# Kernel tuning notes

Measured on AMD Instinct MI355X. Metric: run time of the kernel, lower is better.

The kernel has to match this reference:

```python
import jax, jax.numpy as jnp
import numpy as np

B, S, D, H, F = 2, 2048, 768, 12, 3072
HD = D // H


def setup_inputs() -> dict:
    key = jax.random.key(0)
    ks = jax.random.split(key, 6)
    g = lambda k, sh, sc: jax.random.normal(k, sh, jnp.float32) * sc
    return {
        "x": g(ks[0], (B, S, D), 1.0),
        "mask": jnp.tril(jnp.ones((1, 1, S, S), dtype=jnp.bool_)),  # causal
        "qkv_w": g(ks[1], (3 * D, D), 0.02),
        "qkv_b": jnp.zeros((3 * D,), jnp.float32),
        "out_w": g(ks[2], (D, D), 0.02),
        "out_b": jnp.zeros((D,), jnp.float32),
        "fc1_w": g(ks[3], (F, D), 0.02),
        "fc1_b": jnp.zeros((F,), jnp.float32),
        "fc2_w": g(ks[4], (D, F), 0.02),
        "fc2_b": jnp.zeros((D,), jnp.float32),
        "ln1_w": jnp.ones((D,), jnp.float32),
        "ln1_b": jnp.zeros((D,), jnp.float32),
        "ln2_w": jnp.ones((D,), jnp.float32),
        "ln2_b": jnp.zeros((D,), jnp.float32),
    }


def _layernorm(x, w, b, eps=1e-5):
    m = x.mean(-1, keepdims=True)
    v = ((x - m) ** 2).mean(-1, keepdims=True)
    return (x - m) * jax.lax.rsqrt(v + eps) * w + b


def reference(x, mask, qkv_w, qkv_b, out_w, out_b, fc1_w, fc1_b, fc2_w, fc2_b,
              ln1_w, ln1_b, ln2_w, ln2_b):
    b, s, d = x.shape
    h = d // HD  # num_heads
    # --- pre-norm multi-head self-attention (dropout = eval/identity) ---
    hx = _layernorm(x, ln1_w, ln1_b)
    qkv = hx @ qkv_w.T + qkv_b                      # [b,s,3d]
    qkv = qkv.reshape(b, s, 3, h, HD).transpose(2, 0, 3, 1, 4)  # [3,b,h,s,hd]
    q, k, v = qkv[0], qkv[1], qkv[2]
    scale = jnp.sqrt(jnp.float32(HD))
    scores = jnp.einsum("bhqd,bhkd->bhqk", q, k) / scale  # [b,h,s,s]
    scores = jnp.where(mask, scores, -jnp.inf)
    attn = jax.nn.softmax(scores, axis=-1)
    o = jnp.einsum("bhqk,bhkd->bhqd", attn, v)      # [b,h,s,hd]
    o = o.transpose(0, 2, 1, 3).reshape(b, s, d)
    x = x + (o @ out_w.T + out_b)
    # --- pre-norm GELU feed-forward ---
    h2 = _layernorm(x, ln2_w, ln2_b)
    ff = jax.nn.gelu(h2 @ fc1_w.T + fc1_b, approximate=False) @ fc2_w.T + fc2_b
    return x + ff
```

## Files before the change

kernel.cpp:

```cpp
#include <hip/hip_runtime.h>
#include <hip/hip_bf16.h>
#include <cstdint>
#include <cstddef>

typedef __bf16 bf16;
typedef unsigned short ushort_t;
typedef __attribute__((ext_vector_type(8))) __bf16 bf16x8;
typedef __attribute__((ext_vector_type(4))) __bf16 bf16x4;
typedef __attribute__((ext_vector_type(4))) float f32x4;

#define NB 2
#define NS 2048
#define ND 768
#define NH 12
#define NF 3072
#define NT (NB * NS)

__device__ __forceinline__ f32x4 mfma16(bf16x8 a, bf16x8 b, f32x4 c) {
  return __builtin_amdgcn_mfma_f32_16x16x32_bf16(a, b, c, 0, 0, 0);
}

__device__ __forceinline__ void gl_lds16(const bf16* g, bf16* l) {
  __builtin_amdgcn_global_load_lds(
      (__attribute__((address_space(1))) void*)(uintptr_t)g,
      (__attribute__((address_space(3))) void*)l,
      16, 0, 0);
}

__device__ __forceinline__ int xcd_swz(int lin, int nwg) {
  const int q = nwg >> 3, r = nwg & 7;
  const int x = lin & 7, i = lin >> 3;
  return (x < r ? x * (q + 1) : r * (q + 1) + (x - r) * q) + i;
}

__device__ __forceinline__ float gelu_fast(float v) {
  const float u = v * (0.7978845608028654f + 0.03567740814f * v * v);
  const float e = exp2f(u * 2.885390081777927f);
  return v - v / (1.f + e);
}

__global__ __launch_bounds__(256) void sniff_kernel(
    const ushort_t* __restrict__ x, int* __restrict__ flag) {
  __shared__ int s[4];
  int bad = 0;
  for (int i = threadIdx.x; i < 4096; i += 256) {
    const int e = (x[i] >> 7) & 0xFF;
    bad |= (e >= 0xC0);
  }
  bad = __any(bad) ? 1 : 0;
  if ((threadIdx.x & 63) == 0) s[threadIdx.x >> 6] = bad;
  __syncthreads();
  if (threadIdx.x == 0) *flag = s[0] | s[1] | s[2] | s[3];
}

struct CvtArgs {
  const void* s[8];
  bf16* d[8];
  int n8[8];
  int total8;
};

__global__ __launch_bounds__(256) void cvt_all(CvtArgs a,
                                               const int* __restrict__ flag) {
  const int isf = *flag;
  const int stride = gridDim.x * 256;
  for (int i = blockIdx.x * 256 + threadIdx.x; i < a.total8; i += stride) {
    int seg = 0, off = i;
    while (off >= a.n8[seg]) { off -= a.n8[seg]; ++seg; }
    bf16x8 o;
    if (isf) {
      const float* s = (const float*)a.s[seg] + (size_t)off * 8;
      const f32x4 f0 = *(const f32x4*)s;
      const f32x4 f1 = *(const f32x4*)(s + 4);
#pragma unroll
      for (int j = 0; j < 4; ++j) {
        o[j] = (bf16)f0[j];
        o[4 + j] = (bf16)f1[j];
      }
    } else {
      o = *((const bf16x8*)a.s[seg] + off);
    }
    *((bf16x8*)a.d[seg] + off) = o;
  }
}

__global__ __launch_bounds__(256) void ln_kernel(
    const void* __restrict__ xv, const void* __restrict__ wv,
    const void* __restrict__ bv, bf16* __restrict__ y,
    const int* __restrict__ flag) {
  const int isf = *flag;
  const int row = blockIdx.x * 4 + (threadIdx.x >> 6);
  const int L = threadIdx.x & 63;
  const float* xf = (const float*)xv;
  const bf16* xh = (const bf16*)xv;
  const float* wf = (const float*)wv;
  const bf16* wh = (const bf16*)wv;
  const float* bf_ = (const float*)bv;
  const bf16* bh = (const bf16*)bv;
  const size_t base = (size_t)row * ND;
  float v[12];
  float s = 0.f, s2 = 0.f;
#pragma unroll
  for (int i = 0; i < 12; ++i) {
    const int c = L + i * 64;
    v[i] = isf ? xf[base + c] : (float)xh[base + c];
    s += v[i];
    s2 += v[i] * v[i];
  }
#pragma unroll
  for (int off = 1; off < 64; off <<= 1) {
    s += __shfl_xor(s, off);
    s2 += __shfl_xor(s2, off);
  }
  const float mean = s * (1.f / 768.f);
  const float var = s2 * (1.f / 768.f) - mean * mean;
  const float rstd = rsqrtf(var + 1e-5f);
  bf16* yr = y + base;
#pragma unroll
  for (int i = 0; i < 12; ++i) {
    const int c = L + i * 64;
    const float ww = isf ? wf[c] : (float)wh[c];
    const float bb = isf ? bf_[c] : (float)bh[c];
    yr[c] = (bf16)((v[i] - mean) * rstd * ww + bb);
  }
}

__global__ __launch_bounds__(256) void vt_kernel(
    const bf16* __restrict__ qkv, bf16* __restrict__ vT) {
  const int bh = blockIdx.y;
  const int b = bh / NH, h = bh % NH;
  const int st = blockIdx.x;
  __shared__ bf16 Vs[64 * 72];
  const int tid = threadIdx.x;
  {
    const int r = tid >> 2, c = (tid & 3) * 16;
    const bf16* src =
        qkv + (size_t)(b * NS + st * 64 + r) * (3 * ND) + 2 * ND + h * 64 + c;
    *(bf16x8*)&Vs[r * 72 + c] = *(const bf16x8*)src;
    *(bf16x8*)&Vs[r * 72 + c + 8] = *(const bf16x8*)(src + 8);
  }
  __syncthreads();
  {
    const int hd = tid >> 2, t0 = (tid & 3) * 16;
    bf16x8 o0, o1;
#pragma unroll
    for (int j = 0; j < 8; ++j) {
      o0[j] = Vs[(t0 + j) * 72 + hd];
      o1[j] = Vs[(t0 + 8 + j) * 72 + hd];
    }
    bf16* dst = vT + ((size_t)bh * 64 + hd) * NS + st * 64 + t0;
    *(bf16x8*)dst = o0;
    *(bf16x8*)(dst + 8) = o1;
  }
}

template <int EPI, int TM>
__global__ __launch_bounds__(256) void gemm_fast(
    const bf16* __restrict__ A, const bf16* __restrict__ Bt,
    const bf16* __restrict__ bias, const void* resid, void* C,
    int N, int K, int row0, const int* __restrict__ flag) {
  constexpr int NBUF = (TM == 64) ? 5 : 3;
  constexpr int LOOK = NBUF - 2;
  constexpr int MT = TM / 32;
  __shared__ bf16 As[NBUF][TM * 32];
  __shared__ bf16 Bs[NBUF][128 * 32];
  int isf = 0;
  if (EPI == 2) {
    isf = *flag;
    asm volatile("" ::"s"(isf));
  }
  const int tid = threadIdx.x;
  const int w = tid >> 6, L = tid & 63;
  const int lg = L >> 4, lc = L & 15;
  const int lgx = (lg ^ ((lc >> 1) & 3)) * 8;
  const int wm = (w >> 1) * (TM / 2), wn = (w & 1) * 64;
  const int nwg = gridDim.x * gridDim.y;
  const int lin = xcd_swz(blockIdx.y * gridDim.x + blockIdx.x, nwg);
  const int bm = lin / gridDim.x, bn = lin % gridDim.x;

  const bf16* Ab = A + (size_t)bm * TM * K;
  const bf16* Bb = Bt + (size_t)bn * 128 * K;

  const int sr = tid >> 2;
  const int sc = ((tid & 3) ^ ((tid >> 3) & 3)) * 8;

  f32x4 acc[MT][4];
#pragma unroll
  for (int i = 0; i < MT; ++i)
#pragma unroll
    for (int j = 0; j < 4; ++j) acc[i][j] = (f32x4){0.f, 0.f, 0.f, 0.f};

#define GF_STAGE(buf, kk)                                                   \
  do {                                                                      \
    gl_lds16(Ab + (size_t)sr * K + (kk) + sc, As[buf] + tid * 8);           \
    if (TM == 128)                                                          \
      gl_lds16(Ab + (size_t)(sr + 64) * K + (kk) + sc,                      \
               As[buf] + 2048 + tid * 8);                                   \
    gl_lds16(Bb + (size_t)sr * K + (kk) + sc, Bs[buf] + tid * 8);           \
    gl_lds16(Bb + (size_t)(sr + 64) * K + (kk) + sc,                        \
             Bs[buf] + 2048 + tid * 8);                                     \
  } while (0)

#define GF_COMP(cb)                                                         \
  do {                                                                      \
    bf16x8 af[MT], bfr[4];                                                  \
    _Pragma("unroll") for (int mt = 0; mt < MT; ++mt) af[mt] =              \
        *(const bf16x8*)&As[cb][(wm + mt * 16 + lc) * 32 + lgx];            \
    _Pragma("unroll") for (int nt = 0; nt < 4; ++nt) bfr[nt] =              \
        *(const bf16x8*)&Bs[cb][(wn + nt * 16 + lc) * 32 + lgx];            \
    _Pragma("unroll") for (int mt = 0; mt < MT; ++mt)                       \
        _Pragma("unroll") for (int nt = 0; nt < 4; ++nt) acc[mt][nt] =      \
            mfma16(af[mt], bfr[nt], acc[mt][nt]);                           \
  } while (0)

  const int nk = K >> 5;
#pragma unroll
  for (int s = 0; s < LOOK; ++s)
    if (s < nk) GF_STAGE(s, s * 32);
  int cur = 0, stg = LOOK;
  int k = 0;
  const int kmain = (nk > LOOK) ? nk - LOOK : 0;
  for (; k < kmain; ++k) {
    GF_STAGE(stg, (k + LOOK) * 32);
    if (TM == 64)
      asm volatile("s_waitcnt vmcnt(9)" ::: "memory");
    else
      asm volatile("s_waitcnt vmcnt(4)" ::: "memory");
    asm volatile("s_barrier" ::: "memory");
    GF_COMP(cur);
    cur = (cur + 1 == NBUF) ? 0 : cur + 1;
    stg = (stg + 1 == NBUF) ? 0 : stg + 1;
  }
  __syncthreads();
  for (; k < nk; ++k) {
    GF_COMP(cur);
    cur = (cur + 1 == NBUF) ? 0 : cur + 1;
  }
#undef GF_STAGE
#undef GF_COMP

  const float* rf = (const float*)resid;
  const bf16* rh = (const bf16*)resid;
  float* Cf = (float*)C;
  bf16* Ch = (bf16*)C;
#pragma unroll
  for (int mt = 0; mt < MT; ++mt) {
#pragma unroll
    for (int nt = 0; nt < 4; ++nt) {
      const int col = bn * 128 + wn + nt * 16 + lc;
      const float bv = (float)bias[col];
#pragma unroll
      for (int r = 0; r < 4; ++r) {
        const int row = bm * TM + wm + mt * 16 + lg * 4 + r;
        float v = acc[mt][nt][r] + bv;
        if (EPI == 1) v = gelu_fast(v);
        const size_t idx = (size_t)(row0 + row) * N + col;
        if (EPI == 2) {
          v += isf ? rf[idx] : (float)rh[idx];
          if (isf) Cf[idx] = v; else Ch[idx] = (bf16)v;
        } else {
          Ch[idx] = (bf16)v;
        }
      }
    }
  }
}

__global__ __launch_bounds__(256) void gemm_qkv(
    const bf16* __restrict__ A, const bf16* __restrict__ Bt,
    const bf16* __restrict__ bias, bf16* __restrict__ qkvout,
    bf16* __restrict__ vT) {
  const int K = ND, N = 3 * ND;
  constexpr int NBUF = 3;
  constexpr int LOOK = 1;
  __shared__ bf16 As[NBUF][128 * 32];
  __shared__ bf16 Bs[NBUF][128 * 32];
  const int tid = threadIdx.x;
  const int w = tid >> 6, L = tid & 63;
  const int lg = L >> 4, lc = L & 15;
  const int lgx = (lg ^ ((lc >> 1) & 3)) * 8;
  const int wm = (w >> 1) * 64, wn = (w & 1) * 64;
  const int nwg = gridDim.x * gridDim.y;
  const int lin = xcd_swz(blockIdx.y * gridDim.x + blockIdx.x, nwg);
  const int bm = lin / gridDim.x, bn = lin % gridDim.x;

  const bf16* Ab = A + (size_t)bm * 128 * K;
  const bf16* Bb = Bt + (size_t)bn * 128 * K;

  const int sr = tid >> 2;
  const int sc = ((tid & 3) ^ ((tid >> 3) & 3)) * 8;

  f32x4 acc[4][4];
#pragma unroll
  for (int i = 0; i < 4; ++i)
#pragma unroll
    for (int j = 0; j < 4; ++j) acc[i][j] = (f32x4){0.f, 0.f, 0.f, 0.f};

#define QKV_STAGE(buf, kk)                                                  \
  do {                                                                      \
    gl_lds16(Ab + (size_t)sr * K + (kk) + sc, As[buf] + tid * 8);           \
    gl_lds16(Ab + (size_t)(sr + 64) * K + (kk) + sc,                        \
             As[buf] + 2048 + tid * 8);                                     \
    gl_lds16(Bb + (size_t)sr * K + (kk) + sc, Bs[buf] + tid * 8);           \
    gl_lds16(Bb + (size_t)(sr + 64) * K + (kk) + sc,                        \
             Bs[buf] + 2048 + tid * 8);                                     \
  } while (0)

#define QKV_COMP(cb)                                                        \
  do {                                                                      \
    bf16x8 af[4], bfr[4];                                                   \
    _Pragma("unroll") for (int mt = 0; mt < 4; ++mt) af[mt] =               \
        *(const bf16x8*)&As[cb][(wm + mt * 16 + lc) * 32 + lgx];            \
    _Pragma("unroll") for (int nt = 0; nt < 4; ++nt) bfr[nt] =              \
        *(const bf16x8*)&Bs[cb][(wn + nt * 16 + lc) * 32 + lgx];            \
    _Pragma("unroll") for (int mt = 0; mt < 4; ++mt)                        \
        _Pragma("unroll") for (int nt = 0; nt < 4; ++nt) acc[mt][nt] =      \
            mfma16(af[mt], bfr[nt], acc[mt][nt]);                           \
  } while (0)

  const int nk = K >> 5;
  QKV_STAGE(0, 0);
  int cur = 0, stg = LOOK;
  int k = 0;
  const int kmain = nk - LOOK;
  for (; k < kmain; ++k) {
    QKV_STAGE(stg, (k + LOOK) * 32);
    asm volatile("s_waitcnt vmcnt(4)" ::: "memory");
    asm volatile("s_barrier" ::: "memory");
    QKV_COMP(cur);
    cur = (cur + 1 == NBUF) ? 0 : cur + 1;
    stg = (stg + 1 == NBUF) ? 0 : stg + 1;
  }
  __syncthreads();
  for (; k < nk; ++k) {
    QKV_COMP(cur);
    cur = (cur + 1 == NBUF) ? 0 : cur + 1;
  }
#undef QKV_STAGE
#undef QKV_COMP

#pragma unroll
  for (int mt = 0; mt < 4; ++mt) {
#pragma unroll
    for (int nt = 0; nt < 4; ++nt) {
      const int col = bn * 128 + wn + nt * 16 + lc;
      const float bv = (float)bias[col];
      if (col < 2 * ND) {
#pragma unroll
        for (int r = 0; r < 4; ++r) {
          const int row = bm * 128 + wm + mt * 16 + lg * 4 + r;
          qkvout[(size_t)row * N + col] = (bf16)(acc[mt][nt][r] + bv);
        }
      } else {
        const int colv = col - 2 * ND;
        const int h_ = colv >> 6, hd = colv & 63;
        bf16x4 pk;
#pragma unroll
        for (int r = 0; r < 4; ++r) pk[r] = (bf16)(acc[mt][nt][r] + bv);
        const int tok0 = bm * 128 + wm + mt * 16 + lg * 4;
        const int b_ = tok0 >> 11, s0 = tok0 & (NS - 1);
        *(bf16x4*)&vT[((size_t)(b_ * NH + h_) * 64 + hd) * NS + s0] = pk;
      }
    }
  }
}

template <int EPI>
__global__ __launch_bounds__(256) void gemm_bt(
    const bf16* __restrict__ A, const void* __restrict__ Bt,
    const void* __restrict__ bias, const void* resid, void* C,
    int N, int K, int row0, const int* __restrict__ flag) {
  __shared__ bf16 As[128 * 32];
  __shared__ bf16 Bs[128 * 32];
  const int isf = *flag;
  const int tid = threadIdx.x;
  const int w = tid >> 6, L = tid & 63;
  const int lg = L >> 4, lc = L & 15;
  const int wm = (w >> 1) * 64, wn = (w & 1) * 64;
  const int nwg = gridDim.x * gridDim.y;
  const int lin = xcd_swz(blockIdx.y * gridDim.x + blockIdx.x, nwg);
  const int bm = lin / gridDim.x, bn = lin % gridDim.x;

  const bf16* Ab = A + (size_t)bm * 128 * K;
  const bf16* Bth = (const bf16*)Bt + (size_t)bn * 128 * K;
  const float* Btf = (const float*)Bt + (size_t)bn * 128 * K;

  const int sr = tid >> 1;
  const int sc = (tid & 1) * 16;

  f32x4 acc[4][4];
#pragma unroll
  for (int i = 0; i < 4; ++i)
#pragma unroll
    for (int j = 0; j < 4; ++j) acc[i][j] = (f32x4){0.f, 0.f, 0.f, 0.f};

  for (int k0 = 0; k0 < K; k0 += 32) {
    const bf16* ap = Ab + (size_t)sr * K + k0 + sc;
    const bf16x8 a0 = *(const bf16x8*)ap;
    const bf16x8 a1 = *(const bf16x8*)(ap + 8);
    bf16x8 b0, b1;
    if (isf) {
      const float* bp = Btf + (size_t)sr * K + k0 + sc;
      const f32x4 f0 = *(const f32x4*)bp;
      const f32x4 f1 = *(const f32x4*)(bp + 4);
      const f32x4 f2 = *(const f32x4*)(bp + 8);
      const f32x4 f3 = *(const f32x4*)(bp + 12);
#pragma unroll
      for (int j = 0; j < 4; ++j) {
        b0[j] = (bf16)f0[j];
        b0[4 + j] = (bf16)f1[j];
        b1[j] = (bf16)f2[j];
        b1[4 + j] = (bf16)f3[j];
      }
    } else {
      const bf16* bp = Bth + (size_t)sr * K + k0 + sc;
      b0 = *(const bf16x8*)bp;
      b1 = *(const bf16x8*)(bp + 8);
    }
    __syncthreads();
    *(bf16x8*)&As[sr * 32 + sc] = a0;
    *(bf16x8*)&As[sr * 32 + sc + 8] = a1;
    *(bf16x8*)&Bs[sr * 32 + sc] = b0;
    *(bf16x8*)&Bs[sr * 32 + sc + 8] = b1;
    __syncthreads();

    bf16x8 af[4], bfr[4];
#pragma unroll
    for (int mt = 0; mt < 4; ++mt)
      af[mt] = *(const bf16x8*)&As[(wm + mt * 16 + lc) * 32 + lg * 8];
#pragma unroll
    for (int nt = 0; nt < 4; ++nt)
      bfr[nt] = *(const bf16x8*)&Bs[(wn + nt * 16 + lc) * 32 + lg * 8];
#pragma unroll
    for (int mt = 0; mt < 4; ++mt)
#pragma unroll
      for (int nt = 0; nt < 4; ++nt)
        acc[mt][nt] = mfma16(af[mt], bfr[nt], acc[mt][nt]);
  }

  const float* biasf = (const float*)bias;
  const bf16* biash = (const bf16*)bias;
  const float* rf = (const float*)resid;
  const bf16* rh = (const bf16*)resid;
  float* Cf = (float*)C;
  bf16* Ch = (bf16*)C;
#pragma unroll
  for (int mt = 0; mt < 4; ++mt) {
#pragma unroll
    for (int nt = 0; nt < 4; ++nt) {
      const int col = bn * 128 + wn + nt * 16 + lc;
      const float bv = isf ? biasf[col] : (float)biash[col];
#pragma unroll
      for (int r = 0; r < 4; ++r) {
        const int row = bm * 128 + wm + mt * 16 + lg * 4 + r;
        float v = acc[mt][nt][r] + bv;
        if (EPI == 1) v = gelu_fast(v);
        const size_t idx = (size_t)(row0 + row) * N + col;
        if (EPI == 2) {
          v += isf ? rf[idx] : (float)rh[idx];
          if (isf) Cf[idx] = v; else Ch[idx] = (bf16)v;
        } else {
          Ch[idx] = (bf16)v;
        }
      }
    }
  }
}

__global__ __launch_bounds__(256) void flash_attn_v7(
    const bf16* __restrict__ qkv, const bf16* __restrict__ vT,
    bf16* __restrict__ o) {
  const int nwg = gridDim.x * gridDim.y;
  const int lin = xcd_swz(blockIdx.y * gridDim.x + blockIdx.x, nwg);
  const int bh = lin / gridDim.x;
  const int b = bh / NH, h = bh % NH;
  const int qt = gridDim.x - 1 - (lin % gridDim.x);
  const int q0 = qt * 64;
  const int tid = threadIdx.x;
  const int w = tid >> 6, L = tid & 63;
  const int lg = L >> 4, lc = L & 15;

  __shared__ bf16 Ks[2][64 * 72];
  __shared__ bf16 Vts[2][64 * 72];
  __shared__ bf16 Ps[4][16 * 72];

  const float QSCALE = 0.18033688011112042f;
  const size_t tokq = (size_t)(b * NS + q0 + w * 16 + lc);
  const bf16* qp = qkv + tokq * (3 * ND) + h * 64 + lg * 8;
  bf16x8 qf0, qf1;
  {
    const bf16x8 qr0 = *(const bf16x8*)qp;
    const bf16x8 qr1 = *(const bf16x8*)(qp + 32);
#pragma unroll
    for (int j = 0; j < 8; ++j) {
      qf0[j] = (bf16)((float)qr0[j] * QSCALE);
      qf1[j] = (bf16)((float)qr1[j] * QSCALE);
    }
  }

  const int kr = tid >> 2, kc = (tid & 3) * 16;
  const bf16* kbase =
      qkv + (size_t)(b * NS + kr) * (3 * ND) + ND + h * 64 + kc;
  const bf16* vbase = vT + ((size_t)bh * 64 + kr) * NS + kc;

  f32x4 oacc[4];
#pragma unroll
  for (int nt = 0; nt < 4; ++nt) oacc[nt] = (f32x4){0.f, 0.f, 0.f, 0.f};
  float lacc = 0.f;

  const int nkt = qt + 1;

  bf16x8 kreg[2], vreg[2];
#pragma unroll
  for (int p = 0; p < 2; ++p) {
    kreg[p] = *(const bf16x8*)(kbase + p * 8);
    vreg[p] = *(const bf16x8*)(vbase + p * 8);
  }
  *(bf16x8*)&Ks[0][kr * 72 + kc] = kreg[0];
  *(bf16x8*)&Ks[0][kr * 72 + kc + 8] = kreg[1];
  *(bf16x8*)&Vts[0][kr * 72 + kc] = vreg[0];
  *(bf16x8*)&Vts[0][kr * 72 + kc + 8] = vreg[1];

  for (int kt = 0; kt < nkt; ++kt) {
    __syncthreads();
    const int cur = kt & 1;

    if (kt + 1 < nkt) {
      const bf16* kn = kbase + (size_t)(kt + 1) * 64 * (3 * ND);
      const bf16* vn = vbase + (size_t)(kt + 1) * 64;
#pragma unroll
      for (int p = 0; p < 2; ++p) {
        kreg[p] = *(const bf16x8*)(kn + p * 8);
        vreg[p] = *(const bf16x8*)(vn + p * 8);
      }
    }

    f32x4 s[4];
    __builtin_amdgcn_s_setprio(1);
#pragma unroll
    for (int nt = 0; nt < 4; ++nt) {
      const bf16x8 kb0 =
          *(const bf16x8*)&Ks[cur][(nt * 16 + lc) * 72 + lg * 8];
      const bf16x8 kb1 =
          *(const bf16x8*)&Ks[cur][(nt * 16 + lc) * 72 + 32 + lg * 8];
      f32x4 z = (f32x4){0.f, 0.f, 0.f, 0.f};
      s[nt] = mfma16(kb0, qf0, z);
      s[nt] = mfma16(kb1, qf1, s[nt]);
    }
    __builtin_amdgcn_s_setprio(0);
    if (kt == nkt - 1) {
#pragma unroll
      for (int nt = 0; nt < 4; ++nt)
#pragma unroll
        for (int r = 0; r < 4; ++r) {
          const int kv = nt * 16 + lg * 4 + r;
          const int qrow = w * 16 + lc;
          if (kv > qrow) s[nt][r] = -1.0e30f;
        }
    }
#pragma unroll
    for (int nt = 0; nt < 4; ++nt) {
      bf16x4 pk;
#pragma unroll
      for (int r = 0; r < 4; ++r) {
        const float p = exp2f(fminf(s[nt][r], 20.f));
        lacc += p;
        pk[r] = (bf16)p;
      }
      *(bf16x4*)&Ps[w][lc * 72 + nt * 16 + lg * 4] = pk;
    }
    const bf16x8 pa0 = *(const bf16x8*)&Ps[w][lc * 72 + lg * 8];
    const bf16x8 pa1 = *(const bf16x8*)&Ps[w][lc * 72 + 32 + lg * 8];
    __builtin_amdgcn_s_setprio(1);
#pragma unroll
    for (int nt = 0; nt < 4; ++nt) {
      const bf16x8 v0 =
          *(const bf16x8*)&Vts[cur][(nt * 16 + lc) * 72 + lg * 8];
      const bf16x8 v1 =
          *(const bf16x8*)&Vts[cur][(nt * 16 + lc) * 72 + 32 + lg * 8];
      oacc[nt] = mfma16(pa0, v0, oacc[nt]);
      oacc[nt] = mfma16(pa1, v1, oacc[nt]);
    }
    __builtin_amdgcn_s_setprio(0);

    if (kt + 1 < nkt) {
      const int nxt = cur ^ 1;
      *(bf16x8*)&Ks[nxt][kr * 72 + kc] = kreg[0];
      *(bf16x8*)&Ks[nxt][kr * 72 + kc + 8] = kreg[1];
      *(bf16x8*)&Vts[nxt][kr * 72 + kc] = vreg[0];
      *(bf16x8*)&Vts[nxt][kr * 72 + kc + 8] = vreg[1];
    }
  }

  lacc += __shfl_xor(lacc, 16);
  lacc += __shfl_xor(lacc, 32);
  float lr[4];
#pragma unroll
  for (int r = 0; r < 4; ++r) lr[r] = __shfl(lacc, lg * 4 + r);

#pragma unroll
  for (int nt = 0; nt < 4; ++nt)
#pragma unroll
    for (int r = 0; r < 4; ++r) {
      const int qrow = q0 + w * 16 + lg * 4 + r;
      const float val = oacc[nt][r] / lr[r];
      o[(size_t)(b * NS + qrow) * ND + h * 64 + nt * 16 + lc] = (bf16)val;
    }
}

__global__ __launch_bounds__(256) void flash_attn_v1(
    const bf16* __restrict__ qkv, bf16* __restrict__ o) {
  const int bh = blockIdx.y;
  const int b = bh / NH, h = bh % NH;
  const int qt = gridDim.x - 1 - blockIdx.x;
  const int q0 = qt * 64;
  const int tid = threadIdx.x;
  const int w = tid >> 6, L = tid & 63;
  const int lg = L >> 4, lc = L & 15;

  __shared__ bf16 Ks[64 * 72];
  __shared__ bf16 Vts[64 * 72];
  __shared__ bf16 Ps[4][16 * 72];

  const float QSCALE = 0.18033688011112042f;
  const size_t tokq = (size_t)(b * NS + q0 + w * 16 + lc);
  const bf16* qp = qkv + tokq * (3 * ND) + h * 64 + lg * 8;
  const bf16x8 qr0 = *(const bf16x8*)qp;
  const bf16x8 qr1 = *(const bf16x8*)(qp + 32);
  bf16x8 qf0, qf1;
#pragma unroll
  for (int j = 0; j < 8; ++j) {
    qf0[j] = (bf16)((float)qr0[j] * QSCALE);
    qf1[j] = (bf16)((float)qr1[j] * QSCALE);
  }

  f32x4 oacc[4];
#pragma unroll
  for (int nt = 0; nt < 4; ++nt) oacc[nt] = (f32x4){0.f, 0.f, 0.f, 0.f};
  float lacc[4] = {0.f, 0.f, 0.f, 0.f};

  for (int kt = 0; kt <= qt; ++kt) {
    __syncthreads();
#pragma unroll
    for (int p = 0; p < 2; ++p) {
      const int r = (p * 256 + tid) >> 3;
      const int c = (tid & 7) * 8;
      const bf16* kp =
          qkv + (size_t)(b * NS + kt * 64 + r) * (3 * ND) + ND + h * 64 + c;
      const bf16x8 k8 = *(const bf16x8*)kp;
      *(bf16x8*)&Ks[r * 72 + c] = k8;
      const bf16x8 v8 = *(const bf16x8*)(kp + ND);
#pragma unroll
      for (int j = 0; j < 8; ++j) Vts[(c + j) * 72 + r] = v8[j];
    }
    __syncthreads();

    f32x4 s[4];
#pragma unroll
    for (int nt = 0; nt < 4; ++nt) {
      const bf16x8 b0 = *(const bf16x8*)&Ks[(nt * 16 + lc) * 72 + lg * 8];
      const bf16x8 b1 = *(const bf16x8*)&Ks[(nt * 16 + lc) * 72 + 32 + lg * 8];
      f32x4 z = (f32x4){0.f, 0.f, 0.f, 0.f};
      s[nt] = mfma16(qf0, b0, z);
      s[nt] = mfma16(qf1, b1, s[nt]);
    }
    if (kt == qt) {
#pragma unroll
      for (int nt = 0; nt < 4; ++nt)
#pragma unroll
        for (int r = 0; r < 4; ++r) {
          const int qrow = w * 16 + lg * 4 + r;
          const int kcol = nt * 16 + lc;
          if (kcol > qrow) s[nt][r] = -1.0e30f;
        }
    }
#pragma unroll
    for (int nt = 0; nt < 4; ++nt)
#pragma unroll
      for (int r = 0; r < 4; ++r) {
        const float p = exp2f(fminf(s[nt][r], 20.f));
        lacc[r] += p;
        Ps[w][(lg * 4 + r) * 72 + nt * 16 + lc] = (bf16)p;
      }
    __syncthreads();

    const bf16x8 p0 = *(const bf16x8*)&Ps[w][lc * 72 + lg * 8];
    const bf16x8 p1 = *(const bf16x8*)&Ps[w][lc * 72 + 32 + lg * 8];
#pragma unroll
    for (int nt = 0; nt < 4; ++nt) {
      const bf16x8 v0 = *(const bf16x8*)&Vts[(nt * 16 + lc) * 72 + lg * 8];
      const bf16x8 v1 = *(const bf16x8*)&Vts[(nt * 16 + lc) * 72 + 32 + lg * 8];
      oacc[nt] = mfma16(p0, v0, oacc[nt]);
      oacc[nt] = mfma16(p1, v1, oacc[nt]);
    }
  }

#pragma unroll
  for (int msk = 1; msk < 16; msk <<= 1)
#pragma unroll
    for (int r = 0; r < 4; ++r) lacc[r] += __shfl_xor(lacc[r], msk);

#pragma unroll
  for (int nt = 0; nt < 4; ++nt)
#pragma unroll
    for (int r = 0; r < 4; ++r) {
      const int qrow = q0 + w * 16 + lg * 4 + r;
      const float val = oacc[nt][r] / lacc[r];
      o[(size_t)(b * NS + qrow) * ND + h * 64 + nt * 16 + lc] = (bf16)val;
    }
}

extern "C" void kernel_launch(void* const* d_in, const int* in_sizes, int n_in,
                              void* d_out, int out_size, void* d_ws,
                              size_t ws_size, hipStream_t stream) {
  const void* x = d_in[0];
  const void* qkv_w = d_in[2];
  const void* qkv_b = d_in[3];
  const void* out_w = d_in[4];
  const void* out_b = d_in[5];
  const void* fc1_w = d_in[6];
  const void* fc1_b = d_in[7];
  const void* fc2_w = d_in[8];
  const void* fc2_b = d_in[9];
  const void* ln1_w = d_in[10];
  const void* ln1_b = d_in[11];
  const void* ln2_w = d_in[12];
  const void* ln2_b = d_in[13];
  (void)in_sizes; (void)n_in; (void)out_size;

  char* ws = (char*)d_ws;
  int* flag = (int*)ws;

  sniff_kernel<<<dim3(1), 256, 0, stream>>>((const ushort_t*)x, flag);

  const size_t T1 = 58210048, T2 = 51918592, T3 = 45627136, T4 = 39335680;

  if (ws_size >= T2) {
    bf16* wq = (bf16*)(ws + 256);
    bf16* wo = wq + 1769472;
    bf16* w1 = wo + 589824;
    bf16* w2 = w1 + 2359296;
    bf16* bq = w2 + 2359296;
    bf16* bo = bq + 2304;
    bf16* b1 = bo + 768;
    bf16* b2 = b1 + 3072;
    bf16* slotA = b2 + 768;
    bf16* vT = slotA + (size_t)NT * ND;
    bf16* slotB = vT + (size_t)NT * ND;
    bf16* hx = slotA, *oat = slotA, *h2 = slotA;
    bf16* qkv = slotB;

    CvtArgs ca;
    ca.s[0] = qkv_w; ca.d[0] = wq; ca.n8[0] = 1769472 / 8;
    ca.s[1] = out_w; ca.d[1] = wo; ca.n8[1] = 589824 / 8;
    ca.s[2] = fc1_w; ca.d[2] = w1; ca.n8[2] = 2359296 / 8;
    ca.s[3] = fc2_w; ca.d[3] = w2; ca.n8[3] = 2359296 / 8;
    ca.s[4] = qkv_b; ca.d[4] = bq; ca.n8[4] = 2304 / 8;
    ca.s[5] = out_b; ca.d[5] = bo; ca.n8[5] = 768 / 8;
    ca.s[6] = fc1_b; ca.d[6] = b1; ca.n8[6] = 3072 / 8;
    ca.s[7] = fc2_b; ca.d[7] = b2; ca.n8[7] = 768 / 8;
    ca.total8 = (1769472 + 589824 + 2359296 + 2359296 + 2304 + 768 + 3072 +
                 768) / 8;
    cvt_all<<<dim3(880), 256, 0, stream>>>(ca, flag);

    ln_kernel<<<dim3(NT / 4), 256, 0, stream>>>(x, ln1_w, ln1_b, hx, flag);
    gemm_qkv<<<dim3(18, 32), 256, 0, stream>>>(hx, wq, bq, qkv, vT);
    flash_attn_v7<<<dim3(NS / 64, NB * NH), 256, 0, stream>>>(qkv, vT, oat);
    gemm_fast<2, 64><<<dim3(6, 64), 256, 0, stream>>>(
        oat, wo, bo, x, d_out, ND, ND, 0, flag);
    ln_kernel<<<dim3(NT / 4), 256, 0, stream>>>(d_out, ln2_w, ln2_b, h2, flag);
    if (ws_size >= T1) {
      bf16* ff1 = slotB;
      gemm_fast<1, 128><<<dim3(24, 32), 256, 0, stream>>>(
          h2, w1, b1, nullptr, ff1, NF, ND, 0, flag);
      gemm_fast<2, 64><<<dim3(6, 64), 256, 0, stream>>>(
          ff1, w2, b2, d_out, d_out, ND, NF, 0, flag);
    } else {
      bf16* ff1c = slotB;
      for (int c = 0; c < 2; ++c) {
        gemm_fast<1, 128><<<dim3(24, 16), 256, 0, stream>>>(
            h2 + (size_t)c * 2048 * ND, w1, b1, nullptr, ff1c, NF, ND, 0, flag);
        gemm_fast<2, 64><<<dim3(6, 32), 256, 0, stream>>>(
            ff1c, w2, b2, d_out, d_out, ND, NF, c * 2048, flag);
      }
    }
  } else if (ws_size >= T4) {
    bf16* wq = (bf16*)(ws + 256);
    bf16* wo = wq + 1769472;
    bf16* w1 = wo + 589824;
    bf16* w2 = w1 + 2359296;
    bf16* bq = w2 + 2359296;
    bf16* bo = bq + 2304;
    bf16* b1 = bo + 768;
    bf16* b2 = b1 + 3072;
    bf16* slotA = b2 + 768;
    bf16* slotB = slotA + (size_t)NT * ND;
    bf16* hx = slotA, *oat = slotA, *h2 = slotA;
    bf16* qkv = slotB;

    CvtArgs ca;
    ca.s[0] = qkv_w; ca.d[0] = wq; ca.n8[0] = 1769472 / 8;
    ca.s[1] = out_w; ca.d[1] = wo; ca.n8[1] = 589824 / 8;
    ca.s[2] = fc1_w; ca.d[2] = w1; ca.n8[2] = 2359296 / 8;
    ca.s[3] = fc2_w; ca.d[3] = w2; ca.n8[3] = 2359296 / 8;
    ca.s[4] = qkv_b; ca.d[4] = bq; ca.n8[4] = 2304 / 8;
    ca.s[5] = out_b; ca.d[5] = bo; ca.n8[5] = 768 / 8;
    ca.s[6] = fc1_b; ca.d[6] = b1; ca.n8[6] = 3072 / 8;
    ca.s[7] = fc2_b; ca.d[7] = b2; ca.n8[7] = 768 / 8;
    ca.total8 = (1769472 + 589824 + 2359296 + 2359296 + 2304 + 768 + 3072 +
                 768) / 8;
    cvt_all<<<dim3(880), 256, 0, stream>>>(ca, flag);

    ln_kernel<<<dim3(NT / 4), 256, 0, stream>>>(x, ln1_w, ln1_b, hx, flag);
    gemm_fast<0, 128><<<dim3(18, 32), 256, 0, stream>>>(
        hx, wq, bq, nullptr, qkv, 3 * ND, ND, 0, flag);
    flash_attn_v1<<<dim3(NS / 64, NB * NH), 256, 0, stream>>>(qkv, oat);
    gemm_fast<2, 64><<<dim3(6, 64), 256, 0, stream>>>(
        oat, wo, bo, x, d_out, ND, ND, 0, flag);
    ln_kernel<<<dim3(NT / 4), 256, 0, stream>>>(d_out, ln2_w, ln2_b, h2, flag);
    if (ws_size >= T3) {
      bf16* ff1 = slotB;
      gemm_fast<1, 128><<<dim3(24, 32), 256, 0, stream>>>(
          h2, w1, b1, nullptr, ff1, NF, ND, 0, flag);
      gemm_fast<2, 64><<<dim3(6, 64), 256, 0, stream>>>(
          ff1, w2, b2, d_out, d_out, ND, NF, 0, flag);
    } else {
      bf16* ff1c = slotB;
      for (int c = 0; c < 2; ++c) {
        gemm_fast<1, 128><<<dim3(24, 16), 256, 0, stream>>>(
            h2 + (size_t)c * 2048 * ND, w1, b1, nullptr, ff1c, NF, ND, 0, flag);
        gemm_fast<2, 64><<<dim3(6, 32), 256, 0, stream>>>(
            ff1c, w2, b2, d_out, d_out, ND, NF, c * 2048, flag);
      }
    }
  } else {
    const size_t szTD = (size_t)NT * ND * sizeof(bf16);
    bf16* slotA = (bf16*)(ws + 256);
    bf16* qkv = (bf16*)(ws + 256 + szTD);
    bf16* hx = slotA, *oat = slotA, *h2 = slotA;
    bf16* ff1c = qkv;

    ln_kernel<<<dim3(NT / 4), 256, 0, stream>>>(x, ln1_w, ln1_b, hx, flag);
    gemm_bt<0><<<dim3(18, 32), 256, 0, stream>>>(
        hx, qkv_w, qkv_b, nullptr, qkv, 3 * ND, ND, 0, flag);
    flash_attn_v1<<<dim3(NS / 64, NB * NH), 256, 0, stream>>>(qkv, oat);
    gemm_bt<2><<<dim3(6, 32), 256, 0, stream>>>(
        oat, out_w, out_b, x, d_out, ND, ND, 0, flag);
    ln_kernel<<<dim3(NT / 4), 256, 0, stream>>>(d_out, ln2_w, ln2_b, h2, flag);
    for (int c = 0; c < 4; ++c) {
      gemm_bt<1><<<dim3(24, 8), 256, 0, stream>>>(
          h2 + (size_t)c * 1024 * ND, fc1_w, fc1_b, nullptr, ff1c, NF, ND, 0,
          flag);
      gemm_bt<2><<<dim3(6, 8), 256, 0, stream>>>(
          ff1c, fc2_w, fc2_b, d_out, d_out, ND, NF, c * 1024, flag);
    }
  }
}
```

Baseline: 329.9 us.

## Give each attention wave two query sub-tiles and rebalance causal tile scheduling

The flash attention kernel drops from 4 waves of 16 query rows to 2 waves of 32 rows (128 threads), so each K/V fragment read from LDS feeds two MFMA sub-tiles, halving LDS reads per FLOP. Block-to-(head, q-tile) mapping is replaced with a per-XCD scheme assigning 3 heads per XCD with permuted q-tile orders to balance causal work. The next-tile LDS store is moved before the PV MFMAs. Fewer waves per block and more registers per thread may reduce latency hiding, and the hardcoded 96-per-XCD mapping assumes the current grid shape.

Measured after the change: 336.0 us. Within noise of the previous version (+1.9%).

```diff
diff --git a/kernel.cpp b/kernel.cpp
--- a/kernel.cpp
+++ b/kernel.cpp
@@ -467,14 +467,21 @@
   }
 }
 
-__global__ __launch_bounds__(256) void flash_attn_v7(
+__global__ __launch_bounds__(128) void flash_attn_v7(
     const bf16* __restrict__ qkv, const bf16* __restrict__ vT,
     bf16* __restrict__ o) {
   const int nwg = gridDim.x * gridDim.y;
   const int lin = xcd_swz(blockIdx.y * gridDim.x + blockIdx.x, nwg);
-  const int bh = lin / gridDim.x;
+  const int xcd = lin / 96;
+  const int i96 = lin % 96;
+  const int bl = i96 >> 5;
+  const int j = i96 & 31;
+  const int bh = xcd * 3 + bl;
   const int b = bh / NH, h = bh % NH;
-  const int qt = gridDim.x - 1 - (lin % gridDim.x);
+  int qt;
+  if (bl == 0) qt = j;
+  else if (bl == 1) qt = (j + 16) & 31;
+  else qt = (j < 16) ? (31 - 2 * j) : (62 - 2 * j);
   const int q0 = qt * 64;
   const int tid = threadIdx.x;
   const int w = tid >> 6, L = tid & 63;
@@ -482,44 +489,48 @@
 
   __shared__ bf16 Ks[2][64 * 72];
   __shared__ bf16 Vts[2][64 * 72];
-  __shared__ bf16 Ps[4][16 * 72];
+  __shared__ bf16 Ps[2][32 * 72];
 
   const float QSCALE = 0.18033688011112042f;
-  const size_t tokq = (size_t)(b * NS + q0 + w * 16 + lc);
-  const bf16* qp = qkv + tokq * (3 * ND) + h * 64 + lg * 8;
-  bf16x8 qf0, qf1;
-  {
-    const bf16x8 qr0 = *(const bf16x8*)qp;
-    const bf16x8 qr1 = *(const bf16x8*)(qp + 32);
-#pragma unroll
-    for (int j = 0; j < 8; ++j) {
-      qf0[j] = (bf16)((float)qr0[j] * QSCALE);
-      qf1[j] = (bf16)((float)qr1[j] * QSCALE);
-    }
-  }
-
-  const int kr = tid >> 2, kc = (tid & 3) * 16;
+  bf16x8 qf[2][2];
+#pragma unroll
+  for (int m = 0; m < 2; ++m) {
+    const size_t tokq = (size_t)(b * NS + q0 + w * 32 + m * 16 + lc);
+    const bf16* qp = qkv + tokq * (3 * ND) + h * 64 + lg * 8;
+    const bf16x8 q0r = *(const bf16x8*)qp;
+    const bf16x8 q1r = *(const bf16x8*)(qp + 32);
+#pragma unroll
+    for (int jj = 0; jj < 8; ++jj) {
+      qf[m][0][jj] = (bf16)((float)q0r[jj] * QSCALE);
+      qf[m][1][jj] = (bf16)((float)q1r[jj] * QSCALE);
+    }
+  }
+
+  const int kr = tid >> 1, kc = (tid & 1) * 32;
   const bf16* kbase =
       qkv + (size_t)(b * NS + kr) * (3 * ND) + ND + h * 64 + kc;
   const bf16* vbase = vT + ((size_t)bh * 64 + kr) * NS + kc;
 
-  f32x4 oacc[4];
-#pragma unroll
-  for (int nt = 0; nt < 4; ++nt) oacc[nt] = (f32x4){0.f, 0.f, 0.f, 0.f};
-  float lacc = 0.f;
+  f32x4 oacc[2][4];
+#pragma unroll
+  for (int m = 0; m < 2; ++m)
+#pragma unroll
+    for (int nt = 0; nt < 4; ++nt) oacc[m][nt] = (f32x4){0.f, 0.f, 0.f, 0.f};
+  float lacc[2] = {0.f, 0.f};
 
   const int nkt = qt + 1;
 
-  bf16x8 kreg[2], vreg[2];
-#pragma unroll
-  for (int p = 0; p < 2; ++p) {
+  bf16x8 kreg[4], vreg[4];
+#pragma unroll
+  for (int p = 0; p < 4; ++p) {
     kreg[p] = *(const bf16x8*)(kbase + p * 8);
     vreg[p] = *(const bf16x8*)(vbase + p * 8);
   }
-  *(bf16x8*)&Ks[0][kr * 72 + kc] = kreg[0];
-  *(bf16x8*)&Ks[0][kr * 72 + kc + 8] = kreg[1];
-  *(bf16x8*)&Vts[0][kr * 72 + kc] = vreg[0];
-  *(bf16x8*)&Vts[0][kr * 72 + kc + 8] = vreg[1];
+#pragma unroll
+  for (int p = 0; p < 4; ++p) {
+    *(bf16x8*)&Ks[0][kr * 72 + kc + p * 8] = kreg[p];
+    *(bf16x8*)&Vts[0][kr * 72 + kc + p * 8] = vreg[p];
+  }
 
   for (int kt = 0; kt < nkt; ++kt) {
     __syncthreads();
@@ -529,13 +540,13 @@
       const bf16* kn = kbase + (size_t)(kt + 1) * 64 * (3 * ND);
       const bf16* vn = vbase + (size_t)(kt + 1) * 64;
 #pragma unroll
-      for (int p = 0; p < 2; ++p) {
+      for (int p = 0; p < 4; ++p) {
         kreg[p] = *(const bf16x8*)(kn + p * 8);
         vreg[p] = *(const bf16x8*)(vn + p * 8);
       }
     }
 
-    f32x4 s[4];
+    f32x4 s[2][4];
     __builtin_amdgcn_s_setprio(1);
 #pragma unroll
     for (int nt = 0; nt < 4; ++nt) {
@@ -543,34 +554,55 @@
           *(const bf16x8*)&Ks[cur][(nt * 16 + lc) * 72 + lg * 8];
       const bf16x8 kb1 =
           *(const bf16x8*)&Ks[cur][(nt * 16 + lc) * 72 + 32 + lg * 8];
-      f32x4 z = (f32x4){0.f, 0.f, 0.f, 0.f};
-      s[nt] = mfma16(kb0, qf0, z);
-      s[nt] = mfma16(kb1, qf1, s[nt]);
+#pragma unroll
+      for (int m = 0; m < 2; ++m) {
+        f32x4 z = (f32x4){0.f, 0.f, 0.f, 0.f};
+        s[m][nt] = mfma16(kb0, qf[m][0], z);
+        s[m][nt] = mfma16(kb1, qf[m][1], s[m][nt]);
+      }
     }
     __builtin_amdgcn_s_setprio(0);
     if (kt == nkt - 1) {
 #pragma unroll
-      for (int nt = 0; nt < 4; ++nt)
+      for (int m = 0; m < 2; ++m)
+#pragma unroll
+        for (int nt = 0; nt < 4; ++nt)
+#pragma unroll
+          for (int r = 0; r < 4; ++r) {
+            const int kv = nt * 16 + lg * 4 + r;
+            const int qrow = w * 32 + m * 16 + lc;
+            if (kv > qrow) s[m][nt][r] = -1.0e30f;
+          }
+    }
+#pragma unroll
+    for (int m = 0; m < 2; ++m)
+#pragma unroll
+      for (int nt = 0; nt < 4; ++nt) {
+        bf16x4 pk;
 #pragma unroll
         for (int r = 0; r < 4; ++r) {
-          const int kv = nt * 16 + lg * 4 + r;
-          const int qrow = w * 16 + lc;
-          if (kv > qrow) s[nt][r] = -1.0e30f;
+          const float p = exp2f(fminf(s[m][nt][r], 20.f));
+          lacc[m] += p;
+          pk[r] = (bf16)p;
         }
-    }
-#pragma unroll
-    for (int nt = 0; nt < 4; ++nt) {
-      bf16x4 pk;
-#pragma unroll
-      for (int r = 0; r < 4; ++r) {
-        const float p = exp2f(fminf(s[nt][r], 20.f));
-        lacc += p;
-        pk[r] = (bf16)p;
-      }
-      *(bf16x4*)&Ps[w][lc * 72 + nt * 16 + lg * 4] = pk;
-    }
-    const bf16x8 pa0 = *(const bf16x8*)&Ps[w][lc * 72 + lg * 8];
-    const bf16x8 pa1 = *(const bf16x8*)&Ps[w][lc * 72 + 32 + lg * 8];
+        *(bf16x4*)&Ps[w][(m * 16 + lc) * 72 + nt * 16 + lg * 4] = pk;
+      }
+    bf16x8 pa[2][2];
+#pragma unroll
+    for (int m = 0; m < 2; ++m) {
+      pa[m][0] = *(const bf16x8*)&Ps[w][(m * 16 + lc) * 72 + lg * 8];
+      pa[m][1] = *(const bf16x8*)&Ps[w][(m * 16 + lc) * 72 + 32 + lg * 8];
+    }
+
+    if (kt + 1 < nkt) {
+      const int nxt = cur ^ 1;
+#pragma unroll
+      for (int p = 0; p < 4; ++p) {
+        *(bf16x8*)&Ks[nxt][kr * 72 + kc + p * 8] = kreg[p];
+        *(bf16x8*)&Vts[nxt][kr * 72 + kc + p * 8] = vreg[p];
+      }
+    }
+
     __builtin_amdgcn_s_setprio(1);
 #pragma unroll
     for (int nt = 0; nt < 4; ++nt) {
@@ -578,34 +610,36 @@
           *(const bf16x8*)&Vts[cur][(nt * 16 + lc) * 72 + lg * 8];
       const bf16x8 v1 =
           *(const bf16x8*)&Vts[cur][(nt * 16 + lc) * 72 + 32 + lg * 8];
-      oacc[nt] = mfma16(pa0, v0, oacc[nt]);
-      oacc[nt] = mfma16(pa1, v1, oacc[nt]);
+#pragma unroll
+      for (int m = 0; m < 2; ++m) {
+        oacc[m][nt] = mfma16(pa[m][0], v0, oacc[m][nt]);
+        oacc[m][nt] = mfma16(pa[m][1], v1, oacc[m][nt]);
+      }
     }
     __builtin_amdgcn_s_setprio(0);
-
-    if (kt + 1 < nkt) {
-      const int nxt = cur ^ 1;
-      *(bf16x8*)&Ks[nxt][kr * 72 + kc] = kreg[0];
-      *(bf16x8*)&Ks[nxt][kr * 72 + kc + 8] = kreg[1];
-      *(bf16x8*)&Vts[nxt][kr * 72 + kc] = vreg[0];
-      *(bf16x8*)&Vts[nxt][kr * 72 + kc + 8] = vreg[1];
-    }
-  }
-
-  lacc += __shfl_xor(lacc, 16);
-  lacc += __shfl_xor(lacc, 32);
-  float lr[4];
-#pragma unroll
-  for (int r = 0; r < 4; ++r) lr[r] = __shfl(lacc, lg * 4 + r);
-
-#pragma unroll
-  for (int nt = 0; nt < 4; ++nt)
-#pragma unroll
-    for (int r = 0; r < 4; ++r) {
-      const int qrow = q0 + w * 16 + lg * 4 + r;
-      const float val = oacc[nt][r] / lr[r];
-      o[(size_t)(b * NS + qrow) * ND + h * 64 + nt * 16 + lc] = (bf16)val;
-    }
+  }
+
+#pragma unroll
+  for (int m = 0; m < 2; ++m) {
+    lacc[m] += __shfl_xor(lacc[m], 16);
+    lacc[m] += __shfl_xor(lacc[m], 32);
+  }
+  float lr[2][4];
+#pragma unroll
+  for (int m = 0; m < 2; ++m)
+#pragma unroll
+    for (int r = 0; r < 4; ++r) lr[m][r] = __shfl(lacc[m], lg * 4 + r);
+
+#pragma unroll
+  for (int m = 0; m < 2; ++m)
+#pragma unroll
+    for (int nt = 0; nt < 4; ++nt)
+#pragma unroll
+      for (int r = 0; r < 4; ++r) {
+        const int qrow = q0 + w * 32 + m * 16 + lg * 4 + r;
+        const float val = oacc[m][nt][r] / lr[m][r];
+        o[(size_t)(b * NS + qrow) * ND + h * 64 + nt * 16 + lc] = (bf16)val;
+      }
 }
 
 __global__ __launch_bounds__(256) void flash_attn_v1(
@@ -765,7 +799,7 @@
 
     ln_kernel<<<dim3(NT / 4), 256, 0, stream>>>(x, ln1_w, ln1_b, hx, flag);
     gemm_qkv<<<dim3(18, 32), 256, 0, stream>>>(hx, wq, bq, qkv, vT);
-    flash_attn_v7<<<dim3(NS / 64, NB * NH), 256, 0, stream>>>(qkv, vT, oat);
+    flash_attn_v7<<<dim3(NS / 64, NB * NH), 128, 0, stream>>>(qkv, vT, oat);
     gemm_fast<2, 64><<<dim3(6, 64), 256, 0, stream>>>(
         oat, wo, bo, x, d_out, ND, ND, 0, flag);
     ln_kernel<<<dim3(NT / 4), 256, 0, stream>>>(d_out, ln2_w, ln2_b, h2, flag);
```
